# Optimization experiments

Measured on AMD Instinct MI355X. Metric: run time of the kernel, lower is better.

Reference implementation:

```python
import jax, jax.numpy as jnp
import numpy as np

B, U, D_DEC, D_ENC = 32, 4096, 512, 512
ATT_UNITS, NUM_HEADS = 512, 4
HEAD_DIM = ATT_UNITS // NUM_HEADS
CONV_FILTERS, CONV_K = 32, 31
INIT = 0.075


def setup_inputs() -> dict:
    key = jax.random.key(0)
    ks = jax.random.split(key, 12)
    u = lambda k, shape: jax.random.uniform(k, shape, jnp.float32, -INIT, INIT)
    return {
        "dec_state": jax.random.normal(ks[0], (B, D_DEC), jnp.float32),
        "enc_state": jax.random.normal(ks[1], (B, U, D_ENC), jnp.float32),
        "prev_attention_weights": jax.random.uniform(ks[2], (B, U), jnp.float32),
        # stacked per-head Dense params
        "Wphi": u(ks[3], (NUM_HEADS, D_DEC, HEAD_DIM)),
        "bphi": jnp.zeros((NUM_HEADS, HEAD_DIM), jnp.float32),
        "Wpsi": u(ks[4], (NUM_HEADS, D_ENC, HEAD_DIM)),
        "bpsi": jnp.zeros((NUM_HEADS, HEAD_DIM), jnp.float32),
        # Conv1D kernel in WIO layout: (kernel_size, in_ch=1, out_ch=32), no bias
        "conv_kernel": jax.random.uniform(ks[5], (CONV_K, 1, CONV_FILTERS), jnp.float32, -0.1, 0.1),
        "Wloc": u(ks[6], (CONV_FILTERS, NUM_HEADS)),
        "Wout": u(ks[7], (NUM_HEADS * D_ENC, ATT_UNITS)),
        "bout": jnp.zeros((ATT_UNITS,), jnp.float32),
    }


def reference(dec_state, enc_state, prev_attention_weights,
              Wphi, bphi, Wpsi, bpsi, conv_kernel, Wloc, Wout, bout):
    # location features: Conv1D(same, no bias) over prev attention weights
    loc_feat = jax.lax.conv_general_dilated(
        prev_attention_weights[:, :, None], conv_kernel,
        window_strides=(1,), padding="SAME",
        dimension_numbers=("NWC", "WIO", "NWC"))            # (B, U, 32)
    loc_bias = loc_feat @ Wloc                                 # (B, U, H)
    loc_bias = jnp.transpose(loc_bias, (0, 2, 1))              # (B, H, U)

    # batched per-head projections (replaces the Python per-head loop)
    phi_s = jnp.einsum("bd,hdk->bhk", dec_state, Wphi) + bphi          # (B, H, hd)
    psi_h = jnp.einsum("bue,hek->bhuk", enc_state, Wpsi) + bpsi[:, None, :]  # (B, H, U, hd)

    energy = jnp.einsum("bhk,bhuk->bhu", phi_s, psi_h) + loc_bias      # (B, H, U)
    attn = jax.nn.softmax(energy, axis=-1)                              # (B, H, U)

    context = jnp.einsum("bhu,bue->bhe", attn, enc_state)               # (B, H, E)
    combined = context.reshape(context.shape[0], -1)                    # (B, H*E)
    context_vector = combined @ Wout + bout                             # (B, ATT_UNITS)
    attention_weights = jnp.mean(attn, axis=1)                          # (B, U)
    return context_vector, attention_weights
```

## Files before the change

kernel.cpp:

```cpp
#include <hip/hip_runtime.h>
#include <math.h>

#define B  32
#define U  4096
#define D  512
#define H  4
#define HD 128
#define CK 31
#define CF 32
#define AU 512

#define BPB    32
#define ROWS_W 32

#define LOG2E 1.4426950408889634f

static __device__ __forceinline__ float readlane_f(float v, int l) {
    return __int_as_float(__builtin_amdgcn_readlane(__float_as_int(v), l));
}
static __device__ __forceinline__ float fast_exp2(float x) {
    return __builtin_amdgcn_exp2f(x);
}

__global__ __launch_bounds__(256) void prep_kernel(
    const float* __restrict__ dec,
    const float* __restrict__ Wphi,
    const float* __restrict__ bphi,
    const float* __restrict__ Wpsi,
    const float* __restrict__ bpsi,
    const float* __restrict__ convk,
    const float* __restrict__ Wloc,
    float* __restrict__ ws_v,
    float* __restrict__ ws_const,
    float* __restrict__ ws_ck)
{
    __shared__ float decs[D];
    __shared__ float phis2[2][HD];
    __shared__ float phis[HD];
    const int b = blockIdx.x / H, h = blockIdx.x % H;
    const int tid = threadIdx.x;

    for (int i = tid; i < D; i += 256) decs[i] = dec[b * D + i];
    __syncthreads();

    {
        const int k = tid & 127, half = tid >> 7;
        const int d0 = half * 256;
        float acc = 0.f;
        const float* wp = Wphi + (size_t)h * D * HD + (size_t)d0 * HD + k;
        #pragma unroll 8
        for (int d = 0; d < 256; ++d) acc += decs[d0 + d] * wp[(size_t)d * HD];
        phis2[half][k] = acc;
    }
    __syncthreads();
    if (tid < HD) phis[tid] = phis2[0][tid] + phis2[1][tid] + bphi[h * HD + tid];
    __syncthreads();

    if (tid == 0) {
        float c = 0.f;
        for (int k = 0; k < HD; ++k) c += phis[k] * bpsi[h * HD + k];
        ws_const[b * H + h] = c * LOG2E;
    }

    for (int e = tid; e < D; e += 256) {
        const float* wq = Wpsi + ((size_t)h * D + e) * HD;
        float acc = 0.f;
        #pragma unroll 8
        for (int k = 0; k < HD; ++k) acc += wq[k] * phis[k];
        ws_v[((size_t)b * H + h) * D + e] = acc * LOG2E;
    }

    if (blockIdx.x == 0 && tid < CK * H) {
        int t = tid / H, hh = tid % H;
        float acc = 0.f;
        for (int f = 0; f < CF; ++f) acc += convk[t * CF + f] * Wloc[f * H + hh];
        ws_ck[t * H + hh] = acc * LOG2E;
    }
}

__global__ __launch_bounds__(256, 4) void fused_pass1(
    const float* __restrict__ enc,
    const float* __restrict__ prevw,
    const float* __restrict__ ws_v,
    const float* __restrict__ ws_const,
    const float* __restrict__ ws_ck,
    float* __restrict__ energy,
    float* __restrict__ pctx,
    float* __restrict__ pms)
{
    const int b    = blockIdx.y;
    const int blk  = blockIdx.x;
    const int tid  = threadIdx.x;
    const int lane = tid & 63;
    const int wave = tid >> 6;
    const int ubase = (blk * 4 + wave) * ROWS_W;

    __shared__ float lctx[4][H][D];
    __shared__ float lms[4][H][2];
    __shared__ float lalpha[H][4];

    float4 v0[H], v1[H];
    #pragma unroll
    for (int h = 0; h < H; ++h) {
        const float* vp = ws_v + ((size_t)b * H + h) * D;
        v0[h] = *(const float4*)(vp + lane * 4);
        v1[h] = *(const float4*)(vp + 256 + lane * 4);
    }
    float ckr[H] = {0.f, 0.f, 0.f, 0.f};
    if (lane < CK) {
        #pragma unroll
        for (int h = 0; h < H; ++h) ckr[h] = ws_ck[lane * H + h];
    }
    float ct[H];
    #pragma unroll
    for (int h = 0; h < H; ++h) ct[h] = ws_const[b * H + h];

    float w0;
    {
        const int gi = ubase - 15 + lane;
        w0 = (gi >= 0 && gi < U) ? prevw[b * U + gi] : 0.f;
    }

    float m0 = -3.402823466e38f, m1 = m0, m2 = m0, m3 = m0;
    float s0 = 0.f, s1 = 0.f, s2 = 0.f, s3 = 0.f;
    float4 z = {0.f, 0.f, 0.f, 0.f};
    float4 c00 = z, c01 = z, c10 = z, c11 = z, c20 = z, c21 = z, c30 = z, c31 = z;

    const bool b16 = (lane & 16) != 0;
    const bool b32 = (lane & 32) != 0;

    const float* encb = enc + ((size_t)b * U + ubase) * D;
    float4 e0 = *(const float4*)(encb + lane * 4);
    float4 e1 = *(const float4*)(encb + 256 + lane * 4);
    float4 n0 = *(const float4*)(encb + D + lane * 4);
    float4 n1 = *(const float4*)(encb + D + 256 + lane * 4);

    for (int r = 0; r < ROWS_W; ++r) {
        float4 q0, q1;
        if (r < ROWS_W - 2) {
            const float* nx = encb + (size_t)(r + 2) * D;
            q0 = *(const float4*)(nx + lane * 4);
            q1 = *(const float4*)(nx + 256 + lane * 4);
        }
        const int u = ubase + r;
        float pw = __int_as_float(
            __builtin_amdgcn_ds_bpermute((r + lane) << 2, __float_as_int(w0)));

        float p0 = pw * ckr[0]
            + e0.x*v0[0].x + e0.y*v0[0].y + e0.z*v0[0].z + e0.w*v0[0].w
            + e1.x*v1[0].x + e1.y*v1[0].y + e1.z*v1[0].z + e1.w*v1[0].w;
        float p1 = pw * ckr[1]
            + e0.x*v0[1].x + e0.y*v0[1].y + e0.z*v0[1].z + e0.w*v0[1].w
            + e1.x*v1[1].x + e1.y*v1[1].y + e1.z*v1[1].z + e1.w*v1[1].w;
        float p2 = pw * ckr[2]
            + e0.x*v0[2].x + e0.y*v0[2].y + e0.z*v0[2].z + e0.w*v0[2].w
            + e1.x*v1[2].x + e1.y*v1[2].y + e1.z*v1[2].z + e1.w*v1[2].w;
        float p3 = pw * ckr[3]
            + e0.x*v0[3].x + e0.y*v0[3].y + e0.z*v0[3].z + e0.w*v0[3].w
            + e1.x*v1[3].x + e1.y*v1[3].y + e1.z*v1[3].z + e1.w*v1[3].w;

        float keepA = b16 ? p1 : p0, sendA = b16 ? p0 : p1;
        float a  = keepA + __shfl_xor(sendA, 16);
        float keepB = b16 ? p3 : p2, sendB = b16 ? p2 : p3;
        float bb = keepB + __shfl_xor(sendB, 16);
        float keepC = b32 ? bb : a, sendC = b32 ? a : bb;
        float c = keepC + __shfl_xor(sendC, 32);
        c += __shfl_xor(c, 1);
        c += __shfl_xor(c, 2);
        c += __shfl_xor(c, 4);
        c += __shfl_xor(c, 8);
        float eh0 = readlane_f(c, 0)  + ct[0];
        float eh1 = readlane_f(c, 16) + ct[1];
        float eh2 = readlane_f(c, 32) + ct[2];
        float eh3 = readlane_f(c, 48) + ct[3];

        if (lane < H) {
            float ev = (lane == 0) ? eh0 : (lane == 1) ? eh1 : (lane == 2) ? eh2 : eh3;
            energy[((size_t)b * H + lane) * U + u] = ev;
        }

        float mn0 = fmaxf(m0, eh0), mn1 = fmaxf(m1, eh1);
        float mn2 = fmaxf(m2, eh2), mn3 = fmaxf(m3, eh3);
        if (mn0 > m0 || mn1 > m1 || mn2 > m2 || mn3 > m3) {
            float a0 = fast_exp2(m0 - mn0), a1 = fast_exp2(m1 - mn1);
            float a2 = fast_exp2(m2 - mn2), a3 = fast_exp2(m3 - mn3);
            s0 *= a0; s1 *= a1; s2 *= a2; s3 *= a3;
            c00.x*=a0; c00.y*=a0; c00.z*=a0; c00.w*=a0; c01.x*=a0; c01.y*=a0; c01.z*=a0; c01.w*=a0;
            c10.x*=a1; c10.y*=a1; c10.z*=a1; c10.w*=a1; c11.x*=a1; c11.y*=a1; c11.z*=a1; c11.w*=a1;
            c20.x*=a2; c20.y*=a2; c20.z*=a2; c20.w*=a2; c21.x*=a2; c21.y*=a2; c21.z*=a2; c21.w*=a2;
            c30.x*=a3; c30.y*=a3; c30.z*=a3; c30.w*=a3; c31.x*=a3; c31.y*=a3; c31.z*=a3; c31.w*=a3;
            m0 = mn0; m1 = mn1; m2 = mn2; m3 = mn3;
        }
        float w0e = fast_exp2(eh0 - m0), w1e = fast_exp2(eh1 - m1);
        float w2e = fast_exp2(eh2 - m2), w3e = fast_exp2(eh3 - m3);
        s0 += w0e; s1 += w1e; s2 += w2e; s3 += w3e;
        c00.x += w0e*e0.x; c00.y += w0e*e0.y; c00.z += w0e*e0.z; c00.w += w0e*e0.w;
        c01.x += w0e*e1.x; c01.y += w0e*e1.y; c01.z += w0e*e1.z; c01.w += w0e*e1.w;
        c10.x += w1e*e0.x; c10.y += w1e*e0.y; c10.z += w1e*e0.z; c10.w += w1e*e0.w;
        c11.x += w1e*e1.x; c11.y += w1e*e1.y; c11.z += w1e*e1.z; c11.w += w1e*e1.w;
        c20.x += w2e*e0.x; c20.y += w2e*e0.y; c20.z += w2e*e0.z; c20.w += w2e*e0.w;
        c21.x += w2e*e1.x; c21.y += w2e*e1.y; c21.z += w2e*e1.z; c21.w += w2e*e1.w;
        c30.x += w3e*e0.x; c30.y += w3e*e0.y; c30.z += w3e*e0.z; c30.w += w3e*e0.w;
        c31.x += w3e*e1.x; c31.y += w3e*e1.y; c31.z += w3e*e1.z; c31.w += w3e*e1.w;

        e0 = n0; e1 = n1; n0 = q0; n1 = q1;
    }

    *(float4*)&lctx[wave][0][lane * 4]       = c00;
    *(float4*)&lctx[wave][0][256 + lane * 4] = c01;
    *(float4*)&lctx[wave][1][lane * 4]       = c10;
    *(float4*)&lctx[wave][1][256 + lane * 4] = c11;
    *(float4*)&lctx[wave][2][lane * 4]       = c20;
    *(float4*)&lctx[wave][2][256 + lane * 4] = c21;
    *(float4*)&lctx[wave][3][lane * 4]       = c30;
    *(float4*)&lctx[wave][3][256 + lane * 4] = c31;
    if (lane == 0) {
        lms[wave][0][0] = m0; lms[wave][0][1] = s0;
        lms[wave][1][0] = m1; lms[wave][1][1] = s1;
        lms[wave][2][0] = m2; lms[wave][2][1] = s2;
        lms[wave][3][0] = m3; lms[wave][3][1] = s3;
    }
    __syncthreads();

    const size_t pbase = ((size_t)(b * BPB + blk)) * H;
    if (tid < H) {
        const int h = tid;
        float M = fmaxf(fmaxf(lms[0][h][0], lms[1][h][0]),
                        fmaxf(lms[2][h][0], lms[3][h][0]));
        float S = 0.f;
        #pragma unroll
        for (int w = 0; w < 4; ++w) {
            float al = fast_exp2(lms[w][h][0] - M);
            lalpha[h][w] = al;
            S += al * lms[w][h][1];
        }
        pms[(pbase + h) * 2]     = M;
        pms[(pbase + h) * 2 + 1] = S;
    }
    __syncthreads();

    #pragma unroll
    for (int h = 0; h < H; ++h) {
        const float a0 = lalpha[h][0], a1 = lalpha[h][1];
        const float a2 = lalpha[h][2], a3 = lalpha[h][3];
        #pragma unroll
        for (int half = 0; half < 2; ++half) {
            const int d = tid + half * 256;
            float val = a0 * lctx[0][h][d] + a1 * lctx[1][h][d]
                      + a2 * lctx[2][h][d] + a3 * lctx[3][h][d];
            pctx[(pbase + h) * D + d] = val;
        }
    }
}

__global__ __launch_bounds__(256) void combine_kernel(
    const float* __restrict__ pctx,
    const float* __restrict__ pms,
    float* __restrict__ ctx,
    float* __restrict__ MS)
{
    const int bh = blockIdx.x;
    const int b = bh >> 2, h = bh & 3;
    const int tid = threadIdx.x;
    __shared__ float sm[BPB], ss[BPB], salpha[BPB];
    __shared__ float MSsh[2];

    if (tid < BPB) {
        sm[tid] = pms[(((size_t)b * BPB + tid) * H + h) * 2];
        ss[tid] = pms[(((size_t)b * BPB + tid) * H + h) * 2 + 1];
    }
    __syncthreads();
    if (tid == 0) {
        float M = -3.402823466e38f;
        for (int i = 0; i < BPB; ++i) M = fmaxf(M, sm[i]);
        float S = 0.f;
        for (int i = 0; i < BPB; ++i) {
            float al = fast_exp2(sm[i] - M);
            salpha[i] = al;
            S += al * ss[i];
        }
        MSsh[0] = M; MSsh[1] = S;
        MS[bh * 2] = M; MS[bh * 2 + 1] = S;
    }
    __syncthreads();
    const float invS = 1.0f / MSsh[1];

    float acc0 = 0.f, acc1 = 0.f;
    const float* base = pctx + ((size_t)b * BPB * H + h) * D;
    #pragma unroll 4
    for (int i = 0; i < BPB; ++i) {
        float al = salpha[i];
        const float* p = base + (size_t)i * H * D;
        acc0 += al * p[tid];
        acc1 += al * p[tid + 256];
    }
    ctx[(size_t)bh * D + tid]       = acc0 * invS;
    ctx[(size_t)bh * D + tid + 256] = acc1 * invS;
}

__global__ __launch_bounds__(256) void tail_kernel(
    const float* __restrict__ energy,
    const float* __restrict__ MS,
    const float* __restrict__ ctx,
    const float* __restrict__ Wout,
    const float* __restrict__ bout,
    float* __restrict__ attw,
    float* __restrict__ outv)
{
    const int b = blockIdx.x;
    const int role = blockIdx.y;
    const int tid = threadIdx.x;

    if (role < 16) {
        const int u = role * 256 + tid;
        float acc = 0.f;
        #pragma unroll
        for (int h = 0; h < H; ++h) {
            const float M  = MS[(b * H + h) * 2];
            const float iS = 1.0f / MS[(b * H + h) * 2 + 1];
            acc += fast_exp2(energy[((size_t)b * H + h) * U + u] - M) * iS;
        }
        attw[(size_t)b * U + u] = acc * 0.25f;
    } else {
        const int idx = role - 16;
        const int jh  = idx & 1;
        const int kc  = idx >> 1;
        const int j   = jh * 256 + tid;
        const int i0  = kc * 256;
        __shared__ float c_s[256];
        c_s[tid] = ctx[(size_t)b * (H * D) + i0 + tid];
        __syncthreads();

        float acc = (kc == 0) ? bout[j] : 0.f;
        #pragma unroll 8
        for (int i = 0; i < 256; ++i)
            acc += c_s[i] * Wout[(size_t)(i0 + i) * AU + j];
        atomicAdd(&outv[(size_t)b * AU + j], acc);
    }
}

extern "C" void kernel_launch(void* const* d_in, const int* in_sizes, int n_in,
                              void* d_out, int out_size, void* d_ws, size_t ws_size,
                              hipStream_t stream) {
    const float* dec   = (const float*)d_in[0];
    const float* enc   = (const float*)d_in[1];
    const float* prevw = (const float*)d_in[2];
    const float* Wphi  = (const float*)d_in[3];
    const float* bphi  = (const float*)d_in[4];
    const float* Wpsi  = (const float*)d_in[5];
    const float* bpsi  = (const float*)d_in[6];
    const float* convk = (const float*)d_in[7];
    const float* Wloc  = (const float*)d_in[8];
    const float* Wout  = (const float*)d_in[9];
    const float* bout  = (const float*)d_in[10];

    float* out  = (float*)d_out;
    float* outv = out;
    float* attw = out + B * AU;

    float* ws        = (float*)d_ws;
    float* ws_v      = ws;
    float* ws_const  = ws + 65536;
    float* ws_ck     = ws + 65664;
    float* ws_energy = ws + 65792;
    float* ws_pctx   = ws_energy + (size_t)B*H*U;
    float* ws_pms    = ws_pctx + (size_t)B*BPB*H*D;
    float* ws_MS     = ws_pms + (size_t)B*BPB*H*2;
    float* ws_ctx    = ws_MS + 256;

    hipMemsetAsync(outv, 0, (size_t)B * AU * sizeof(float), stream);

    prep_kernel<<<dim3(B * H), 256, 0, stream>>>(dec, Wphi, bphi, Wpsi, bpsi,
                                                 convk, Wloc, ws_v, ws_const, ws_ck);
    fused_pass1<<<dim3(BPB, B), 256, 0, stream>>>(enc, prevw, ws_v, ws_const,
                                                  ws_ck, ws_energy, ws_pctx, ws_pms);
    combine_kernel<<<dim3(B * H), 256, 0, stream>>>(ws_pctx, ws_pms, ws_ctx, ws_MS);
    tail_kernel<<<dim3(B, 32), 256, 0, stream>>>(ws_energy, ws_MS, ws_ctx,
                                                 Wout, bout, attw, outv);
}
```

Measured before the change: 435.6 us.

## Fuse combine into pass1 via last-block atomic counter, drop memset

Folds the cross-block softmax/context combine into the main pass: each block bumps a per-batch atomic counter, and the last block to finish does the max/sum merge and context reduction. The output zeroing moves from a separate memset into the prep kernel, along with the counter reset. The Wpsi dot product is also vectorised with float4 loads. This removes two launches and their gaps, at the cost of a serialized tail inside the last block per batch and extra shared memory that may reduce occupancy.

After: 576.4 us. 1.32x slower.

```diff
diff --git a/kernel.cpp b/kernel.cpp
--- a/kernel.cpp
+++ b/kernel.cpp
@@ -32,13 +32,18 @@
     const float* __restrict__ Wloc,
     float* __restrict__ ws_v,
     float* __restrict__ ws_const,
-    float* __restrict__ ws_ck)
+    float* __restrict__ ws_ck,
+    float* __restrict__ outv,
+    int*   __restrict__ cnt)
 {
     __shared__ float decs[D];
     __shared__ float phis2[2][HD];
     __shared__ float phis[HD];
     const int b = blockIdx.x / H, h = blockIdx.x % H;
     const int tid = threadIdx.x;
+
+    if (tid < 128) outv[(size_t)b * AU + h * 128 + tid] = 0.f;
+    if (blockIdx.x == 0 && tid >= 128 && tid < 128 + B) cnt[tid - 128] = 0;
 
     for (int i = tid; i < D; i += 256) decs[i] = dec[b * D + i];
     __syncthreads();
@@ -63,10 +68,14 @@
     }
 
     for (int e = tid; e < D; e += 256) {
-        const float* wq = Wpsi + ((size_t)h * D + e) * HD;
+        const float4* wq = (const float4*)(Wpsi + ((size_t)h * D + e) * HD);
         float acc = 0.f;
         #pragma unroll 8
-        for (int k = 0; k < HD; ++k) acc += wq[k] * phis[k];
+        for (int k = 0; k < HD / 4; ++k) {
+            float4 w = wq[k];
+            acc += w.x * phis[4*k] + w.y * phis[4*k+1]
+                 + w.z * phis[4*k+2] + w.w * phis[4*k+3];
+        }
         ws_v[((size_t)b * H + h) * D + e] = acc * LOG2E;
     }
 
@@ -86,7 +95,10 @@
     const float* __restrict__ ws_ck,
     float* __restrict__ energy,
     float* __restrict__ pctx,
-    float* __restrict__ pms)
+    float* __restrict__ pms,
+    float* __restrict__ ctx,
+    float* __restrict__ MS,
+    int*   __restrict__ cnt)
 {
     const int b    = blockIdx.y;
     const int blk  = blockIdx.x;
@@ -98,6 +110,9 @@
     __shared__ float lctx[4][H][D];
     __shared__ float lms[4][H][2];
     __shared__ float lalpha[H][4];
+    __shared__ float csm[H][BPB], css[H][BPB], csal[H][BPB];
+    __shared__ float cMS[H][2];
+    __shared__ int lastflag;
 
     float4 v0[H], v1[H];
     #pragma unroll
@@ -135,6 +150,8 @@
     float4 n0 = *(const float4*)(encb + D + lane * 4);
     float4 n1 = *(const float4*)(encb + D + 256 + lane * 4);
 
+    float* ep = energy + ((size_t)b * H + (lane < H ? lane : 0)) * U + ubase;
+
     for (int r = 0; r < ROWS_W; ++r) {
         float4 q0, q1;
         if (r < ROWS_W - 2) {
@@ -142,7 +159,6 @@
             q0 = *(const float4*)(nx + lane * 4);
             q1 = *(const float4*)(nx + 256 + lane * 4);
         }
-        const int u = ubase + r;
         float pw = __int_as_float(
             __builtin_amdgcn_ds_bpermute((r + lane) << 2, __float_as_int(w0)));
 
@@ -176,7 +192,7 @@
 
         if (lane < H) {
             float ev = (lane == 0) ? eh0 : (lane == 1) ? eh1 : (lane == 2) ? eh2 : eh3;
-            energy[((size_t)b * H + lane) * U + u] = ev;
+            ep[r] = ev;
         }
 
         float mn0 = fmaxf(m0, eh0), mn1 = fmaxf(m1, eh1);
@@ -251,51 +267,52 @@
             pctx[(pbase + h) * D + d] = val;
         }
     }
-}
-
-__global__ __launch_bounds__(256) void combine_kernel(
-    const float* __restrict__ pctx,
-    const float* __restrict__ pms,
-    float* __restrict__ ctx,
-    float* __restrict__ MS)
-{
-    const int bh = blockIdx.x;
-    const int b = bh >> 2, h = bh & 3;
-    const int tid = threadIdx.x;
-    __shared__ float sm[BPB], ss[BPB], salpha[BPB];
-    __shared__ float MSsh[2];
-
-    if (tid < BPB) {
-        sm[tid] = pms[(((size_t)b * BPB + tid) * H + h) * 2];
-        ss[tid] = pms[(((size_t)b * BPB + tid) * H + h) * 2 + 1];
-    }
-    __syncthreads();
+
+    __threadfence();
     if (tid == 0) {
+        int prev = atomicAdd(&cnt[b], 1);
+        lastflag = (prev == BPB - 1) ? 1 : 0;
+    }
+    __syncthreads();
+    if (!lastflag) return;
+    __threadfence();
+
+    if (tid < 128) {
+        const int i = tid >> 2, h = tid & 3;
+        csm[h][i] = pms[(((size_t)b * BPB + i) * H + h) * 2];
+        css[h][i] = pms[(((size_t)b * BPB + i) * H + h) * 2 + 1];
+    }
+    __syncthreads();
+    if (tid < H) {
+        const int h = tid;
         float M = -3.402823466e38f;
-        for (int i = 0; i < BPB; ++i) M = fmaxf(M, sm[i]);
+        for (int i = 0; i < BPB; ++i) M = fmaxf(M, csm[h][i]);
         float S = 0.f;
         for (int i = 0; i < BPB; ++i) {
-            float al = fast_exp2(sm[i] - M);
-            salpha[i] = al;
-            S += al * ss[i];
-        }
-        MSsh[0] = M; MSsh[1] = S;
-        MS[bh * 2] = M; MS[bh * 2 + 1] = S;
-    }
-    __syncthreads();
-    const float invS = 1.0f / MSsh[1];
-
-    float acc0 = 0.f, acc1 = 0.f;
-    const float* base = pctx + ((size_t)b * BPB * H + h) * D;
-    #pragma unroll 4
-    for (int i = 0; i < BPB; ++i) {
-        float al = salpha[i];
-        const float* p = base + (size_t)i * H * D;
-        acc0 += al * p[tid];
-        acc1 += al * p[tid + 256];
-    }
-    ctx[(size_t)bh * D + tid]       = acc0 * invS;
-    ctx[(size_t)bh * D + tid + 256] = acc1 * invS;
+            float al = fast_exp2(csm[h][i] - M);
+            csal[h][i] = al;
+            S += al * css[h][i];
+        }
+        cMS[h][0] = M; cMS[h][1] = S;
+        MS[(b * H + h) * 2]     = M;
+        MS[(b * H + h) * 2 + 1] = S;
+    }
+    __syncthreads();
+
+    #pragma unroll
+    for (int h = 0; h < H; ++h) {
+        const float iS = 1.0f / cMS[h][1];
+        #pragma unroll
+        for (int half = 0; half < 2; ++half) {
+            const int d = tid + half * 256;
+            float acc = 0.f;
+            const float* pp = pctx + (((size_t)b * BPB) * H + h) * D + d;
+            #pragma unroll 8
+            for (int i = 0; i < BPB; ++i)
+                acc += csal[h][i] * pp[(size_t)i * H * D];
+            ctx[((size_t)b * H + h) * D + d] = acc * iS;
+        }
+    }
 }
 
 __global__ __launch_bounds__(256) void tail_kernel(
@@ -367,14 +384,14 @@
     float* ws_pms    = ws_pctx + (size_t)B*BPB*H*D;
     float* ws_MS     = ws_pms + (size_t)B*BPB*H*2;
     float* ws_ctx    = ws_MS + 256;
-
-    hipMemsetAsync(outv, 0, (size_t)B * AU * sizeof(float), stream);
+    int*   ws_cnt    = (int*)(ws_ctx + (size_t)B*H*D);
 
     prep_kernel<<<dim3(B * H), 256, 0, stream>>>(dec, Wphi, bphi, Wpsi, bpsi,
-                                                 convk, Wloc, ws_v, ws_const, ws_ck);
+                                                 convk, Wloc, ws_v, ws_const,
+                                                 ws_ck, outv, ws_cnt);
     fused_pass1<<<dim3(BPB, B), 256, 0, stream>>>(enc, prevw, ws_v, ws_const,
-                                                  ws_ck, ws_energy, ws_pctx, ws_pms);
-    combine_kernel<<<dim3(B * H), 256, 0, stream>>>(ws_pctx, ws_pms, ws_ctx, ws_MS);
+                                                  ws_ck, ws_energy, ws_pctx,
+                                                  ws_pms, ws_ctx, ws_MS, ws_cnt);
     tail_kernel<<<dim3(B, 32), 256, 0, stream>>>(ws_energy, ws_MS, ws_ctx,
                                                  Wout, bout, attw, outv);
 }
```
